# Kernel optimization log

Measured on AMD Instinct MI355X. Metric: run time of the kernel, lower is better.

## Reference

```python
import jax, jax.numpy as jnp
import numpy as np

NHEAD = 8
NEG = -1e30


def sine_pos_1d(pad_mask, hidden_dim):
    # PositionEmbeddingSine1D (normalize=True, scale=2*pi, temperature=10000)
    not_mask = (~pad_mask).astype(jnp.float32)
    x_embed = jnp.cumsum(not_mask, axis=1)
    x_embed = x_embed / (x_embed[:, -1:] + 1e-6) * (2.0 * np.pi)
    dim_t = jnp.arange(hidden_dim, dtype=jnp.float32)
    dim_t = 10000.0 ** (2.0 * jnp.floor(dim_t / 2.0) / hidden_dim)
    pos_x = x_embed[:, :, None] / dim_t  # [b, s, c]
    pos = jnp.stack([jnp.sin(pos_x[:, :, 0::2]), jnp.cos(pos_x[:, :, 1::2])], axis=3)
    return pos.reshape(pad_mask.shape[0], pad_mask.shape[1], hidden_dim)  # [b, s, c]


def mha_cross(q_in, k_in, v_in, key_pad_mask, Wqkv, bqkv, Wo, bo):
    # torch nn.MultiheadAttention math, batch-first layout [bt, L, d]
    bt, Lq, d = q_in.shape
    hd = d // NHEAD
    Wq, Wk, Wv = jnp.split(Wqkv, 3, axis=0)
    bq, bk, bv = jnp.split(bqkv, 3)
    q = (q_in @ Wq.T + bq).reshape(bt, Lq, NHEAD, hd)
    k = (k_in @ Wk.T + bk).reshape(bt, -1, NHEAD, hd)
    v = (v_in @ Wv.T + bv).reshape(bt, -1, NHEAD, hd)
    scores = jnp.einsum('bqhd,bkhd->bhqk', q, k) / jnp.sqrt(jnp.float32(hd))
    scores = jnp.where(key_pad_mask[:, None, None, :], NEG, scores)
    attn = jax.nn.softmax(scores, axis=-1)
    out = jnp.einsum('bhqk,bkhd->bqhd', attn, v).reshape(bt, Lq, d)
    return out @ Wo.T + bo


def reference(video_feats_0, video_feats_1, video_feats_2, video_feats_3,
              video_poses_0, video_poses_1, video_poses_2, video_poses_3,
              text_feats, text_pad_masks, amr_feats, amr_pad_masks,
              in_proj_weight, in_proj_bias, out_proj_weight, out_proj_bias):
    BT = video_feats_0.shape[0]
    B = text_feats.shape[0]
    T = BT // B
    C = text_feats.shape[-1]
    # repeat over frames: 'b s c -> (b t) s c'
    tf = jnp.repeat(text_feats, T, axis=0)
    tpm = jnp.repeat(text_pad_masks, T, axis=0)
    af = jnp.repeat(amr_feats, T, axis=0)
    apm = jnp.repeat(amr_pad_masks, T, axis=0)
    text_pos = sine_pos_1d(tpm, C)          # [BT, St, C]
    amr_pos = jnp.zeros_like(af)
    memory = jnp.concatenate([tf, af], axis=1)
    mem_pm = jnp.concatenate([tpm, apm], axis=1)
    mem_pos = jnp.concatenate([text_pos, amr_pos], axis=1)
    k_in = memory + mem_pos

    outs = []
    for feat, pos in [(video_feats_0, video_poses_0), (video_feats_1, video_poses_1),
                      (video_feats_2, video_poses_2), (video_feats_3, video_poses_3)]:
        h, w = feat.shape[-2:]
        x = feat.reshape(BT, C, h * w).transpose(0, 2, 1)   # [BT, HW, C]
        p = pos.reshape(BT, C, h * w).transpose(0, 2, 1)
        tgt2 = mha_cross(x + p, k_in, memory, mem_pm,
                         in_proj_weight, in_proj_bias, out_proj_weight, out_proj_bias)
        gated = x * tgt2                                     # elementwise gate
        outs.append(gated.transpose(0, 2, 1).reshape(BT, C, h, w))
    return tuple(outs)


def setup_inputs() -> dict:
    key = jax.random.key(0)
    ks = jax.random.split(key, 16)
    C, B, T = 256, 2, 8
    BT = B * T
    St, Sa = 30, 40
    sizes = [80, 40, 20, 10]
    inp = {}
    for i, s in enumerate(sizes):
        inp[f'video_feats_{i}'] = jax.random.normal(ks[i], (BT, C, s, s), jnp.float32)
        inp[f'video_poses_{i}'] = jax.random.normal(ks[4 + i], (BT, C, s, s), jnp.float32)
    inp['text_feats'] = jax.random.normal(ks[8], (B, St, C), jnp.float32)
    inp['amr_feats'] = jax.random.normal(ks[9], (B, Sa, C), jnp.float32)
    # pad masks: last few tokens padded (True = padded)
    inp['text_pad_masks'] = jnp.arange(St)[None, :].repeat(B, axis=0) >= (St - 4)
    inp['amr_pad_masks'] = jnp.arange(Sa)[None, :].repeat(B, axis=0) >= (Sa - 6)
    s = 1.0 / np.sqrt(C)
    inp['in_proj_weight'] = jax.random.normal(ks[10], (3 * C, C), jnp.float32) * s
    inp['in_proj_bias'] = jnp.zeros((3 * C,), jnp.float32)
    inp['out_proj_weight'] = jax.random.normal(ks[11], (C, C), jnp.float32) * s
    inp['out_proj_bias'] = jnp.zeros((C,), jnp.float32)
    return inp
```

## Files before the change

kernel.cpp:

```cpp
#include <hip/hip_runtime.h>
#include <math.h>

#define CC 256
#define NH 8
#define HD 32
#define BT 16
#define TQ 32
#define LT 30
#define LA 40
#define ABS 264
#define QS 40
#define PS 72
#define SUB 2304
#define SLICE 4608
#define NEGF -1e30f

typedef __bf16 bf16x8 __attribute__((ext_vector_type(8)));
typedef float floatx4 __attribute__((ext_vector_type(4)));

__device__ inline unsigned short f2bf(float f) {
  unsigned int u = __float_as_uint(f);
  u += 0x7fffu + ((u >> 16) & 1u);
  return (unsigned short)(u >> 16);
}

__global__ __launch_bounds__(256) void prep_all(
    const float* __restrict__ text_feats,
    const float* __restrict__ amr_feats,
    const int*   __restrict__ text_pad,
    const int*   __restrict__ amr_pad,
    const float* __restrict__ in_w,
    const float* __restrict__ in_b,
    const float* __restrict__ out_w,
    unsigned short* __restrict__ wq_pack,
    unsigned short* __restrict__ wo_pack,
    unsigned short* __restrict__ Kc,
    unsigned short* __restrict__ Vt,
    int* __restrict__ nvp) {
  int t = threadIdx.x;
  __shared__ float mem[CC], kin[CC], shx[2];
  __shared__ int sh_l;
  if (blockIdx.x < 64) {
    int idx = blockIdx.x * 256 + t;
    int mm = idx >> 13;
    int r = idx & 8191;
    int lane = r & 63;
    int ks = (r >> 6) & 7;
    int nt = (r >> 9) & 15;
    int row = nt * 16 + (lane & 15);
    int k0 = ks * 32 + (lane >> 4) * 8;
    const float* W = mm ? out_w : in_w;
    unsigned short* dst = (mm ? wo_pack : wq_pack) + (size_t)r * 8;
    #pragma unroll
    for (int j = 0; j < 8; ++j) dst[j] = f2bf(W[row * CC + k0 + j]);
    return;
  }
  int bidx = blockIdx.x - 64;
  int b = bidx >> 6;
  int slot = bidx & 63;
  if (t == 0) {
    int n = 0, l = -1;
    float cum = 0.f, cl = 0.f;
    for (int j = 0; j < LT; ++j) {
      if (!text_pad[b * LT + j]) {
        cum += 1.f;
        if (n == slot) { l = j; cl = cum; }
        n++;
      }
    }
    for (int j = 0; j < LA; ++j) {
      if (!amr_pad[b * LA + j]) {
        if (n == slot) l = LT + j;
        n++;
      }
    }
    sh_l = l;
    shx[0] = cl;
    shx[1] = cum;
    if (slot == 0) nvp[b] = n;
  }
  __syncthreads();
  int l = sh_l;
  float m_ = 0.f, pos = 0.f;
  if (l >= 0) {
    if (l < LT) m_ = text_feats[(b * LT + l) * CC + t];
    else        m_ = amr_feats[(b * LA + (l - LT)) * CC + t];
    if (l < LT) {
      float xh = shx[0] / (shx[1] + 1e-6f) * 6.283185307179586f;
      float i2 = (float)((t >> 1) * 2);
      float dt = powf(10000.0f, i2 / 256.0f);
      float val = xh / dt;
      pos = (t & 1) ? cosf(val) : sinf(val);
    }
  }
  mem[t] = m_;
  kin[t] = m_ + pos;
  __syncthreads();
  unsigned short kout = 0, vout = 0;
  if (l >= 0) {
    const float4* wk4 = (const float4*)(in_w + (size_t)(CC + t) * CC);
    const float4* wv4 = (const float4*)(in_w + (size_t)(2 * CC + t) * CC);
    float ak = in_b[CC + t];
    float av = in_b[2 * CC + t];
    #pragma unroll 4
    for (int c4 = 0; c4 < 64; ++c4) {
      float4 wk = wk4[c4], wv = wv4[c4];
      int c = c4 * 4;
      ak += kin[c] * wk.x + kin[c + 1] * wk.y + kin[c + 2] * wk.z + kin[c + 3] * wk.w;
      av += mem[c] * wv.x + mem[c + 1] * wv.y + mem[c + 2] * wv.z + mem[c + 3] * wv.w;
    }
    kout = f2bf(ak * 0.17677669529663687f);
    vout = f2bf(av);
  }
  Kc[(size_t)(b * 64 + slot) * CC + t] = kout;
  Vt[((size_t)b * CC + t) * 64 + slot] = vout;
}

__device__ inline void mfma_gemm(const unsigned short* __restrict__ Wp,
                                 const unsigned short* Abuf_s,
                                 int w, int lane, floatx4 acc[2][4]) {
  int arow = lane & 15;
  int aq = (lane >> 4) * 8;
  #pragma unroll
  for (int ks = 0; ks < 8; ++ks) {
    bf16x8 a0 = *(const bf16x8*)&Abuf_s[arow * ABS + ks * 32 + aq];
    bf16x8 a1 = *(const bf16x8*)&Abuf_s[(arow + 16) * ABS + ks * 32 + aq];
    #pragma unroll
    for (int ntl = 0; ntl < 4; ++ntl) {
      bf16x8 bb = *(const bf16x8*)(Wp + ((size_t)((w * 4 + ntl) * 8 + ks) * 64 + lane) * 8);
      acc[0][ntl] = __builtin_amdgcn_mfma_f32_16x16x32_bf16(a0, bb, acc[0][ntl], 0, 0, 0);
      acc[1][ntl] = __builtin_amdgcn_mfma_f32_16x16x32_bf16(a1, bb, acc[1][ntl], 0, 0, 0);
    }
  }
}

__device__ inline void store_cols(float* Qb, const float* __restrict__ bias,
                                  int w, int lane, floatx4 acc[2][4]) {
  #pragma unroll
  for (int ntl = 0; ntl < 4; ++ntl) {
    int c = w * 64 + ntl * 16 + (lane & 15);
    float bv = bias[c];
    #pragma unroll
    for (int mt = 0; mt < 2; ++mt) {
      #pragma unroll
      for (int reg = 0; reg < 4; ++reg) {
        int qi = mt * 16 + ((lane >> 4) & 3) * 4 + reg;
        Qb[c * 32 + ((qi + c) & 31)] = acc[mt][ntl][reg] + bv;
      }
    }
  }
}

__global__ __launch_bounds__(256) void attn_main(
    const float* __restrict__ f0, const float* __restrict__ p0,
    const float* __restrict__ f1, const float* __restrict__ p1,
    const float* __restrict__ f2, const float* __restrict__ p2,
    const float* __restrict__ f3, const float* __restrict__ p3,
    const unsigned short* __restrict__ Kc,
    const unsigned short* __restrict__ Vt,
    const unsigned short* __restrict__ wq_pack,
    const unsigned short* __restrict__ wo_pack,
    const float* __restrict__ in_b, const float* __restrict__ out_b,
    const int* __restrict__ nvp, float* __restrict__ out) {
  __shared__ unsigned short Abuf[TQ * ABS];
  __shared__ float Uf[9216];
  unsigned short* Uu = (unsigned short*)Uf;
  int t = threadIdx.x;
  int lane = t & 63;
  int w = t >> 6;
  int blk = blockIdx.x;
  int bt = blk / 267;
  int r = blk - bt * 267;
  const float* xb; const float* pb; float* ob; int HW; int tile;
  if (r < 200)      { HW = 6400; xb = f0; pb = p0; ob = out;            tile = r; }
  else if (r < 250) { HW = 1600; xb = f1; pb = p1; ob = out + 26214400; tile = r - 200; }
  else if (r < 263) { HW = 400;  xb = f2; pb = p2; ob = out + 32768000; tile = r - 250; }
  else              { HW = 100;  xb = f3; pb = p3; ob = out + 34406400; tile = r - 263; }
  size_t base = (size_t)bt * CC * HW;
  xb += base; pb += base; ob += base;
  int q0 = tile * TQ;
  int b = bt >> 3;
  int nv = nvp[b];

  int c0 = t >> 3;
  int qi0 = (t & 7) * 4;

  {
    int pos = q0 + qi0;
    bool ok = pos < HW;
    #pragma unroll
    for (int it = 0; it < 8; ++it) {
      int c = it * 32 + c0;
      float4 xv = make_float4(0.f, 0.f, 0.f, 0.f), pv = xv;
      if (ok) {
        xv = *(const float4*)(xb + (size_t)c * HW + pos);
        pv = *(const float4*)(pb + (size_t)c * HW + pos);
      }
      Abuf[(qi0 + 0) * ABS + c] = f2bf(xv.x + pv.x);
      Abuf[(qi0 + 1) * ABS + c] = f2bf(xv.y + pv.y);
      Abuf[(qi0 + 2) * ABS + c] = f2bf(xv.z + pv.z);
      Abuf[(qi0 + 3) * ABS + c] = f2bf(xv.w + pv.w);
    }
  }
  __syncthreads();

  {
    floatx4 acc[2][4];
    #pragma unroll
    for (int i = 0; i < 2; ++i)
      #pragma unroll
      for (int j = 0; j < 4; ++j) acc[i][j] = (floatx4){0.f, 0.f, 0.f, 0.f};
    mfma_gemm(wq_pack, Abuf, w, lane, acc);
    int m = lane & 15, g = lane >> 4;
    unsigned short* Qs = Uu + w * SLICE;
    #pragma unroll
    for (int ntl = 0; ntl < 4; ++ntl) {
      int cc = ntl * 16 + m;
      float bv = in_b[w * 64 + cc];
      int hh = cc >> 5, d = cc & 31;
      #pragma unroll
      for (int mt = 0; mt < 2; ++mt)
        #pragma unroll
        for (int reg = 0; reg < 4; ++reg)
          Qs[hh * SUB + (mt * 16 + g * 4 + reg) * QS + d] = f2bf(acc[mt][ntl][reg] + bv);
    }
  }
  __syncthreads();

  {
    int m = lane & 15, g = lane >> 4;
    const unsigned short* Kb = Kc + (size_t)b * 16384;
    const unsigned short* Vb = Vt + (size_t)b * 16384;
    unsigned short* Ws = Uu + w * SLICE;
    float msk[4];
    #pragma unroll
    for (int nt = 0; nt < 4; ++nt) msk[nt] = (nt * 16 + m < nv) ? 0.f : NEGF;
    #pragma unroll
    for (int hh = 0; hh < 2; ++hh) {
      int h = w * 2 + hh;
      bf16x8 aq0 = *(const bf16x8*)&Ws[hh * SUB + m * QS + g * 8];
      bf16x8 aq1 = *(const bf16x8*)&Ws[hh * SUB + (16 + m) * QS + g * 8];
      floatx4 s4[2][4];
      #pragma unroll
      for (int nt = 0; nt < 4; ++nt) {
        bf16x8 bk = *(const bf16x8*)&Kb[(size_t)(nt * 16 + m) * CC + h * HD + g * 8];
        s4[0][nt] = __builtin_amdgcn_mfma_f32_16x16x32_bf16(aq0, bk, (floatx4){0.f,0.f,0.f,0.f}, 0, 0, 0);
        s4[1][nt] = __builtin_amdgcn_mfma_f32_16x16x32_bf16(aq1, bk, (floatx4){0.f,0.f,0.f,0.f}, 0, 0, 0);
      }
      #pragma unroll
      for (int mt = 0; mt < 2; ++mt) {
        #pragma unroll
        for (int reg = 0; reg < 4; ++reg) {
          float v0 = s4[mt][0][reg] + msk[0];
          float v1 = s4[mt][1][reg] + msk[1];
          float v2 = s4[mt][2][reg] + msk[2];
          float v3 = s4[mt][3][reg] + msk[3];
          float mx = fmaxf(fmaxf(v0, v1), fmaxf(v2, v3));
          mx = fmaxf(mx, __shfl_xor(mx, 1));
          mx = fmaxf(mx, __shfl_xor(mx, 2));
          mx = fmaxf(mx, __shfl_xor(mx, 4));
          mx = fmaxf(mx, __shfl_xor(mx, 8));
          float e0 = __expf(v0 - mx), e1 = __expf(v1 - mx);
          float e2 = __expf(v2 - mx), e3 = __expf(v3 - mx);
          float sm = (e0 + e1) + (e2 + e3);
          sm += __shfl_xor(sm, 1);
          sm += __shfl_xor(sm, 2);
          sm += __shfl_xor(sm, 4);
          sm += __shfl_xor(sm, 8);
          float inv = 1.f / sm;
          unsigned short* Pr = &Ws[hh * SUB + (mt * 16 + g * 4 + reg) * PS + m];
          Pr[0]  = f2bf(e0 * inv);
          Pr[16] = f2bf(e1 * inv);
          Pr[32] = f2bf(e2 * inv);
          Pr[48] = f2bf(e3 * inv);
        }
      }
      floatx4 o4[2][2];
      #pragma unroll
      for (int mt = 0; mt < 2; ++mt)
        #pragma unroll
        for (int nt = 0; nt < 2; ++nt) o4[mt][nt] = (floatx4){0.f, 0.f, 0.f, 0.f};
      #pragma unroll
      for (int ks = 0; ks < 2; ++ks) {
        bf16x8 pa0 = *(const bf16x8*)&Ws[hh * SUB + m * PS + ks * 32 + g * 8];
        bf16x8 pa1 = *(const bf16x8*)&Ws[hh * SUB + (16 + m) * PS + ks * 32 + g * 8];
        #pragma unroll
        for (int nt = 0; nt < 2; ++nt) {
          bf16x8 bv = *(const bf16x8*)&Vb[(size_t)(h * HD + nt * 16 + m) * 64 + ks * 32 + g * 8];
          o4[0][nt] = __builtin_amdgcn_mfma_f32_16x16x32_bf16(pa0, bv, o4[0][nt], 0, 0, 0);
          o4[1][nt] = __builtin_amdgcn_mfma_f32_16x16x32_bf16(pa1, bv, o4[1][nt], 0, 0, 0);
        }
      }
      #pragma unroll
      for (int mt = 0; mt < 2; ++mt)
        #pragma unroll
        for (int nt = 0; nt < 2; ++nt)
          #pragma unroll
          for (int reg = 0; reg < 4; ++reg)
            Abuf[(mt * 16 + g * 4 + reg) * ABS + w * 64 + hh * HD + nt * 16 + m] =
                f2bf(o4[mt][nt][reg]);
    }
  }
  __syncthreads();

  {
    floatx4 acc[2][4];
    #pragma unroll
    for (int i = 0; i < 2; ++i)
      #pragma unroll
      for (int j = 0; j < 4; ++j) acc[i][j] = (floatx4){0.f, 0.f, 0.f, 0.f};
    mfma_gemm(wo_pack, Abuf, w, lane, acc);
    store_cols(Uf, out_b, w, lane, acc);
  }
  __syncthreads();

  {
    int pos = q0 + qi0;
    if (pos < HW) {
      #pragma unroll
      for (int it = 0; it < 8; ++it) {
        int c = it * 32 + c0;
        float4 xv = *(const float4*)(xb + (size_t)c * HW + pos);
        float4 g;
        g.x = xv.x * Uf[c * 32 + ((qi0 + 0 + c) & 31)];
        g.y = xv.y * Uf[c * 32 + ((qi0 + 1 + c) & 31)];
        g.z = xv.z * Uf[c * 32 + ((qi0 + 2 + c) & 31)];
        g.w = xv.w * Uf[c * 32 + ((qi0 + 3 + c) & 31)];
        *(float4*)(ob + (size_t)c * HW + pos) = g;
      }
    }
  }
}

extern "C" void kernel_launch(void* const* d_in, const int* in_sizes, int n_in,
                              void* d_out, int out_size, void* d_ws, size_t ws_size,
                              hipStream_t stream) {
  const float* f0 = (const float*)d_in[0];
  const float* p0 = (const float*)d_in[1];
  const float* f1 = (const float*)d_in[2];
  const float* p1 = (const float*)d_in[3];
  const float* f2 = (const float*)d_in[4];
  const float* p2 = (const float*)d_in[5];
  const float* f3 = (const float*)d_in[6];
  const float* p3 = (const float*)d_in[7];
  const float* text_feats = (const float*)d_in[8];
  const float* amr_feats  = (const float*)d_in[9];
  const int*   text_pad   = (const int*)d_in[10];
  const int*   amr_pad    = (const int*)d_in[11];
  const float* in_w  = (const float*)d_in[12];
  const float* in_b  = (const float*)d_in[13];
  const float* out_w = (const float*)d_in[14];
  const float* out_b = (const float*)d_in[15];
  float* out = (float*)d_out;

  unsigned short* wq_pack = (unsigned short*)d_ws;
  unsigned short* wo_pack = wq_pack + 65536;
  unsigned short* Kc = wo_pack + 65536;
  unsigned short* Vt = Kc + 32768;
  int* nvp = (int*)(Vt + 32768);

  prep_all<<<192, 256, 0, stream>>>(text_feats, amr_feats, text_pad, amr_pad,
                                    in_w, in_b, out_w, wq_pack, wo_pack,
                                    Kc, Vt, nvp);
  attn_main<<<BT * 267, 256, 0, stream>>>(f0, p0, f1, p1, f2, p2, f3, p3,
                                          Kc, Vt, wq_pack, wo_pack,
                                          in_b, out_b, nvp, out);
}
```

Before: 490.8 us.

## Shrink shared memory, drop max-subtraction and syncs, gate directly from accumulators

Cuts per-block LDS by removing the float staging buffer and packing Q, P and the attention output into one compact per-wave slice, and adds launch_bounds(256,4) to allow more resident blocks. The softmax no longer subtracts the row max and normalizes after the PV product, and P is staged through LDS in halves. The barrier after the Q projection is dropped, and the output projection reads A directly from the wave slices, then gates and stores straight from the MFMA accumulators. Skipping the max subtraction risks overflow for large scores, and the final stores become less coalesced (float4 per lane across channels).

```diff
diff --git a/kernel.cpp b/kernel.cpp
--- a/kernel.cpp
+++ b/kernel.cpp
@@ -9,10 +9,8 @@
 #define LT 30
 #define LA 40
 #define ABS 264
-#define QS 40
-#define PS 72
-#define SUB 2304
-#define SLICE 4608
+#define QR 40
+#define SL 2560
 #define NEGF -1e30f
 
 typedef __bf16 bf16x8 __attribute__((ext_vector_type(8)));
@@ -134,24 +132,7 @@
   }
 }
 
-__device__ inline void store_cols(float* Qb, const float* __restrict__ bias,
-                                  int w, int lane, floatx4 acc[2][4]) {
-  #pragma unroll
-  for (int ntl = 0; ntl < 4; ++ntl) {
-    int c = w * 64 + ntl * 16 + (lane & 15);
-    float bv = bias[c];
-    #pragma unroll
-    for (int mt = 0; mt < 2; ++mt) {
-      #pragma unroll
-      for (int reg = 0; reg < 4; ++reg) {
-        int qi = mt * 16 + ((lane >> 4) & 3) * 4 + reg;
-        Qb[c * 32 + ((qi + c) & 31)] = acc[mt][ntl][reg] + bv;
-      }
-    }
-  }
-}
-
-__global__ __launch_bounds__(256) void attn_main(
+__global__ __launch_bounds__(256, 4) void attn_main(
     const float* __restrict__ f0, const float* __restrict__ p0,
     const float* __restrict__ f1, const float* __restrict__ p1,
     const float* __restrict__ f2, const float* __restrict__ p2,
@@ -162,12 +143,14 @@
     const unsigned short* __restrict__ wo_pack,
     const float* __restrict__ in_b, const float* __restrict__ out_b,
     const int* __restrict__ nvp, float* __restrict__ out) {
-  __shared__ unsigned short Abuf[TQ * ABS];
-  __shared__ float Uf[9216];
-  unsigned short* Uu = (unsigned short*)Uf;
+  __shared__ unsigned short sh[TQ * ABS + 4 * SL];
+  unsigned short* Abuf = sh;
+  unsigned short* Slc = sh + TQ * ABS;
   int t = threadIdx.x;
   int lane = t & 63;
   int w = t >> 6;
+  int m = lane & 15;
+  int g = lane >> 4;
   int blk = blockIdx.x;
   int bt = blk / 267;
   int r = blk - bt * 267;
@@ -211,35 +194,33 @@
       #pragma unroll
       for (int j = 0; j < 4; ++j) acc[i][j] = (floatx4){0.f, 0.f, 0.f, 0.f};
     mfma_gemm(wq_pack, Abuf, w, lane, acc);
-    int m = lane & 15, g = lane >> 4;
-    unsigned short* Qs = Uu + w * SLICE;
+    unsigned short* Ws = Slc + w * SL;
     #pragma unroll
     for (int ntl = 0; ntl < 4; ++ntl) {
-      int cc = ntl * 16 + m;
-      float bv = in_b[w * 64 + cc];
-      int hh = cc >> 5, d = cc & 31;
+      int hh = ntl >> 1;
+      int d = (ntl & 1) * 16 + m;
+      float bv = in_b[w * 64 + ntl * 16 + m];
       #pragma unroll
       for (int mt = 0; mt < 2; ++mt)
         #pragma unroll
         for (int reg = 0; reg < 4; ++reg)
-          Qs[hh * SUB + (mt * 16 + g * 4 + reg) * QS + d] = f2bf(acc[mt][ntl][reg] + bv);
-    }
-  }
-  __syncthreads();
+          Ws[hh * 1280 + (mt * 16 + g * 4 + reg) * QR + d] = f2bf(acc[mt][ntl][reg] + bv);
+    }
+  }
 
   {
-    int m = lane & 15, g = lane >> 4;
     const unsigned short* Kb = Kc + (size_t)b * 16384;
     const unsigned short* Vb = Vt + (size_t)b * 16384;
-    unsigned short* Ws = Uu + w * SLICE;
+    unsigned short* Ws = Slc + w * SL;
     float msk[4];
     #pragma unroll
     for (int nt = 0; nt < 4; ++nt) msk[nt] = (nt * 16 + m < nv) ? 0.f : NEGF;
     #pragma unroll
     for (int hh = 0; hh < 2; ++hh) {
       int h = w * 2 + hh;
-      bf16x8 aq0 = *(const bf16x8*)&Ws[hh * SUB + m * QS + g * 8];
-      bf16x8 aq1 = *(const bf16x8*)&Ws[hh * SUB + (16 + m) * QS + g * 8];
+      unsigned short* R = Ws + hh * 1280;
+      bf16x8 aq0 = *(const bf16x8*)&R[m * QR + g * 8];
+      bf16x8 aq1 = *(const bf16x8*)&R[(16 + m) * QR + g * 8];
       floatx4 s4[2][4];
       #pragma unroll
       for (int nt = 0; nt < 4; ++nt) {
@@ -247,34 +228,24 @@
         s4[0][nt] = __builtin_amdgcn_mfma_f32_16x16x32_bf16(aq0, bk, (floatx4){0.f,0.f,0.f,0.f}, 0, 0, 0);
         s4[1][nt] = __builtin_amdgcn_mfma_f32_16x16x32_bf16(aq1, bk, (floatx4){0.f,0.f,0.f,0.f}, 0, 0, 0);
       }
-      #pragma unroll
-      for (int mt = 0; mt < 2; ++mt) {
+      float sm[2][4];
+      #pragma unroll
+      for (int mt = 0; mt < 2; ++mt)
         #pragma unroll
         for (int reg = 0; reg < 4; ++reg) {
-          float v0 = s4[mt][0][reg] + msk[0];
-          float v1 = s4[mt][1][reg] + msk[1];
-          float v2 = s4[mt][2][reg] + msk[2];
-          float v3 = s4[mt][3][reg] + msk[3];
-          float mx = fmaxf(fmaxf(v0, v1), fmaxf(v2, v3));
-          mx = fmaxf(mx, __shfl_xor(mx, 1));
-          mx = fmaxf(mx, __shfl_xor(mx, 2));
-          mx = fmaxf(mx, __shfl_xor(mx, 4));
-          mx = fmaxf(mx, __shfl_xor(mx, 8));
-          float e0 = __expf(v0 - mx), e1 = __expf(v1 - mx);
-          float e2 = __expf(v2 - mx), e3 = __expf(v3 - mx);
-          float sm = (e0 + e1) + (e2 + e3);
-          sm += __shfl_xor(sm, 1);
-          sm += __shfl_xor(sm, 2);
-          sm += __shfl_xor(sm, 4);
-          sm += __shfl_xor(sm, 8);
-          float inv = 1.f / sm;
-          unsigned short* Pr = &Ws[hh * SUB + (mt * 16 + g * 4 + reg) * PS + m];
-          Pr[0]  = f2bf(e0 * inv);
-          Pr[16] = f2bf(e1 * inv);
-          Pr[32] = f2bf(e2 * inv);
-          Pr[48] = f2bf(e3 * inv);
+          float e0 = __expf(s4[mt][0][reg] + msk[0]);
+          float e1 = __expf(s4[mt][1][reg] + msk[1]);
+          float e2 = __expf(s4[mt][2][reg] + msk[2]);
+          float e3 = __expf(s4[mt][3][reg] + msk[3]);
+          s4[mt][0][reg] = e0; s4[mt][1][reg] = e1;
+          s4[mt][2][reg] = e2; s4[mt][3][reg] = e3;
+          float s_ = (e0 + e1) + (e2 + e3);
+          s_ += __shfl_xor(s_, 1);
+          s_ += __shfl_xor(s_, 2);
+          s_ += __shfl_xor(s_, 4);
+          s_ += __shfl_xor(s_, 8);
+          sm[mt][reg] = s_;
         }
-      }
       floatx4 o4[2][2];
       #pragma unroll
       for (int mt = 0; mt < 2; ++mt)
@@ -282,8 +253,16 @@
         for (int nt = 0; nt < 2; ++nt) o4[mt][nt] = (floatx4){0.f, 0.f, 0.f, 0.f};
       #pragma unroll
       for (int ks = 0; ks < 2; ++ks) {
-        bf16x8 pa0 = *(const bf16x8*)&Ws[hh * SUB + m * PS + ks * 32 + g * 8];
-        bf16x8 pa1 = *(const bf16x8*)&Ws[hh * SUB + (16 + m) * PS + ks * 32 + g * 8];
+        #pragma unroll
+        for (int mt = 0; mt < 2; ++mt)
+          #pragma unroll
+          for (int reg = 0; reg < 4; ++reg) {
+            int row = (mt * 16 + g * 4 + reg) * QR;
+            R[row + m]      = f2bf(s4[mt][2 * ks][reg]);
+            R[row + 16 + m] = f2bf(s4[mt][2 * ks + 1][reg]);
+          }
+        bf16x8 pa0 = *(const bf16x8*)&R[m * QR + g * 8];
+        bf16x8 pa1 = *(const bf16x8*)&R[(16 + m) * QR + g * 8];
         #pragma unroll
         for (int nt = 0; nt < 2; ++nt) {
           bf16x8 bv = *(const bf16x8*)&Vb[(size_t)(h * HD + nt * 16 + m) * 64 + ks * 32 + g * 8];
@@ -294,11 +273,12 @@
       #pragma unroll
       for (int mt = 0; mt < 2; ++mt)
         #pragma unroll
-        for (int nt = 0; nt < 2; ++nt)
-          #pragma unroll
-          for (int reg = 0; reg < 4; ++reg)
-            Abuf[(mt * 16 + g * 4 + reg) * ABS + w * 64 + hh * HD + nt * 16 + m] =
-                f2bf(o4[mt][nt][reg]);
+        for (int reg = 0; reg < 4; ++reg) {
+          float inv = 1.f / sm[mt][reg];
+          int row = (mt * 16 + g * 4 + reg) * QR;
+          R[row + m]      = f2bf(o4[mt][0][reg] * inv);
+          R[row + 16 + m] = f2bf(o4[mt][1][reg] * inv);
+        }
     }
   }
   __syncthreads();
@@ -309,24 +289,34 @@
     for (int i = 0; i < 2; ++i)
       #pragma unroll
       for (int j = 0; j < 4; ++j) acc[i][j] = (floatx4){0.f, 0.f, 0.f, 0.f};
-    mfma_gemm(wo_pack, Abuf, w, lane, acc);
-    store_cols(Uf, out_b, w, lane, acc);
-  }
-  __syncthreads();
-
-  {
-    int pos = q0 + qi0;
-    if (pos < HW) {
-      #pragma unroll
-      for (int it = 0; it < 8; ++it) {
-        int c = it * 32 + c0;
-        float4 xv = *(const float4*)(xb + (size_t)c * HW + pos);
-        float4 g;
-        g.x = xv.x * Uf[c * 32 + ((qi0 + 0 + c) & 31)];
-        g.y = xv.y * Uf[c * 32 + ((qi0 + 1 + c) & 31)];
-        g.z = xv.z * Uf[c * 32 + ((qi0 + 2 + c) & 31)];
-        g.w = xv.w * Uf[c * 32 + ((qi0 + 3 + c) & 31)];
-        *(float4*)(ob + (size_t)c * HW + pos) = g;
+    #pragma unroll
+    for (int ks = 0; ks < 8; ++ks) {
+      const unsigned short* bA = Slc + (ks >> 1) * SL + (ks & 1) * 1280;
+      bf16x8 a0 = *(const bf16x8*)&bA[m * QR + g * 8];
+      bf16x8 a1 = *(const bf16x8*)&bA[(16 + m) * QR + g * 8];
+      #pragma unroll
+      for (int ntl = 0; ntl < 4; ++ntl) {
+        bf16x8 bb = *(const bf16x8*)(wo_pack + ((size_t)((w * 4 + ntl) * 8 + ks) * 64 + lane) * 8);
+        acc[0][ntl] = __builtin_amdgcn_mfma_f32_16x16x32_bf16(a0, bb, acc[0][ntl], 0, 0, 0);
+        acc[1][ntl] = __builtin_amdgcn_mfma_f32_16x16x32_bf16(a1, bb, acc[1][ntl], 0, 0, 0);
+      }
+    }
+    #pragma unroll
+    for (int ntl = 0; ntl < 4; ++ntl) {
+      int c = w * 64 + ntl * 16 + m;
+      float bv = out_b[c];
+      #pragma unroll
+      for (int mt = 0; mt < 2; ++mt) {
+        int pos = q0 + mt * 16 + g * 4;
+        if (pos < HW) {
+          float4 xv = *(const float4*)(xb + (size_t)c * HW + pos);
+          float4 gg;
+          gg.x = xv.x * (acc[mt][ntl][0] + bv);
+          gg.y = xv.y * (acc[mt][ntl][1] + bv);
+          gg.z = xv.z * (acc[mt][ntl][2] + bv);
+          gg.w = xv.w * (acc[mt][ntl][3] + bv);
+          *(float4*)(ob + (size_t)c * HW + pos) = gg;
+        }
       }
     }
   }
```

After: 457.1 us. 1.07x faster.
